# Kernel optimization log

Hardware: AMD Instinct MI355X
Metric: run time of the kernel (lower is better)

The kernel has to match this reference:

```python
import jax, jax.numpy as jnp
import numpy as np

EPS = 1e-6
H = 16  # num_heads


def _layernorm(x):
    m = jnp.mean(x, axis=-1, keepdims=True)
    v = jnp.mean((x - m) ** 2, axis=-1, keepdims=True)
    return (x - m) * jax.lax.rsqrt(v + EPS)


def _rmsnorm(x, scale):
    return x * jax.lax.rsqrt(jnp.mean(x * x, axis=-1, keepdims=True) + EPS) * scale


def _modulation(vec, w, b):
    # vec: [B, D] -> 6 tensors of [B, 1, D]
    out = jax.nn.silu(vec) @ w + b
    return jnp.split(out[:, None, :], 6, axis=-1)


def _qkv_heads(x, w):
    # x: [B, L, D] -> q,k,v each [B, H, L, Dh]  (rearrange 'B L (K H D) -> K B H L D')
    B, L, _ = x.shape
    qkv = (x @ w).reshape(B, L, 3, H, -1)
    qkv = jnp.transpose(qkv, (2, 0, 3, 1, 4))
    return qkv[0], qkv[1], qkv[2]


def _apply_rope(xq, xk, pe):
    # pe: [B, 1, L, Dh//2, 2, 2]
    shp = xq.shape
    xq_ = xq.reshape(*shp[:-1], -1, 1, 2)
    xk_ = xk.reshape(*shp[:-1], -1, 1, 2)
    xq_out = pe[..., 0] * xq_[..., 0] + pe[..., 1] * xq_[..., 1]
    xk_out = pe[..., 0] * xk_[..., 0] + pe[..., 1] * xk_[..., 1]
    return xq_out.reshape(shp), xk_out.reshape(shp)


def _attention(q, k, v, pe):
    q, k = _apply_rope(q, k, pe)
    scale = q.shape[-1] ** -0.5
    logits = jnp.einsum('bhqd,bhkd->bhqk', q, k) * scale
    probs = jax.nn.softmax(logits, axis=-1)
    x = jnp.einsum('bhqk,bhkd->bhqd', probs, v)
    B, h, L, Dh = x.shape
    return jnp.transpose(x, (0, 2, 1, 3)).reshape(B, L, h * Dh)


def reference(obs, cond, vec, pe,
              obs_mod_w, obs_mod_b, obs_qkv_w, obs_q_scale, obs_k_scale,
              obs_proj_w, obs_proj_b, obs_mlp_w1, obs_mlp_b1, obs_mlp_w2, obs_mlp_b2,
              cond_mod_w, cond_mod_b, cond_qkv_w, cond_q_scale, cond_k_scale,
              cond_proj_w, cond_proj_b, cond_mlp_w1, cond_mlp_b1, cond_mlp_w2, cond_mlp_b2):
    o_shift1, o_scale1, o_gate1, o_shift2, o_scale2, o_gate2 = _modulation(vec, obs_mod_w, obs_mod_b)
    c_shift1, c_scale1, c_gate1, c_shift2, c_scale2, c_gate2 = _modulation(vec, cond_mod_w, cond_mod_b)

    obs_m = (1 + o_scale1) * _layernorm(obs) + o_shift1
    oq, ok, ov = _qkv_heads(obs_m, obs_qkv_w)
    oq = _rmsnorm(oq, obs_q_scale)
    ok = _rmsnorm(ok, obs_k_scale)

    cond_m = (1 + c_scale1) * _layernorm(cond) + c_shift1
    cq, ck, cv = _qkv_heads(cond_m, cond_qkv_w)
    cq = _rmsnorm(cq, cond_q_scale)
    ck = _rmsnorm(ck, cond_k_scale)

    q = jnp.concatenate((cq, oq), axis=2)
    k = jnp.concatenate((ck, ok), axis=2)
    v = jnp.concatenate((cv, ov), axis=2)
    attn = _attention(q, k, v, pe)
    Lc = cond.shape[1]
    cond_attn, obs_attn = attn[:, :Lc], attn[:, Lc:]

    obs = obs + o_gate1 * (obs_attn @ obs_proj_w + obs_proj_b)
    h_obs = (1 + o_scale2) * _layernorm(obs) + o_shift2
    obs = obs + o_gate2 * (jax.nn.gelu(h_obs @ obs_mlp_w1 + obs_mlp_b1, approximate=True) @ obs_mlp_w2 + obs_mlp_b2)

    cond = cond + c_gate1 * (cond_attn @ cond_proj_w + cond_proj_b)
    h_cond = (1 + c_scale2) * _layernorm(cond) + c_shift2
    cond = cond + c_gate2 * (jax.nn.gelu(h_cond @ cond_mlp_w1 + cond_mlp_b1, approximate=True) @ cond_mlp_w2 + cond_mlp_b2)
    return obs, cond


def setup_inputs() -> dict:
    key = jax.random.key(0)
    ks = jax.random.split(key, 24)
    D, Dh, Mh = 1024, 64, 4096
    Lo, Lc = 3072, 1024
    B = 1
    s = 0.02
    inp = {
        'obs': jax.random.normal(ks[0], (B, Lo, D), jnp.float32),
        'cond': jax.random.normal(ks[1], (B, Lc, D), jnp.float32),
        'vec': jax.random.normal(ks[2], (B, D), jnp.float32),
        'pe': jax.random.normal(ks[3], (B, 1, Lo + Lc, Dh // 2, 2, 2), jnp.float32),
        'obs_mod_w': jax.random.normal(ks[4], (D, 6 * D), jnp.float32) * s,
        'obs_mod_b': jax.random.normal(ks[5], (6 * D,), jnp.float32) * s,
        'obs_qkv_w': jax.random.normal(ks[6], (D, 3 * D), jnp.float32) * s,
        'obs_q_scale': jnp.ones((Dh,), jnp.float32),
        'obs_k_scale': jnp.ones((Dh,), jnp.float32),
        'obs_proj_w': jax.random.normal(ks[7], (D, D), jnp.float32) * s,
        'obs_proj_b': jax.random.normal(ks[8], (D,), jnp.float32) * s,
        'obs_mlp_w1': jax.random.normal(ks[9], (D, Mh), jnp.float32) * s,
        'obs_mlp_b1': jax.random.normal(ks[10], (Mh,), jnp.float32) * s,
        'obs_mlp_w2': jax.random.normal(ks[11], (Mh, D), jnp.float32) * s,
        'obs_mlp_b2': jax.random.normal(ks[12], (D,), jnp.float32) * s,
        'cond_mod_w': jax.random.normal(ks[13], (D, 6 * D), jnp.float32) * s,
        'cond_mod_b': jax.random.normal(ks[14], (6 * D,), jnp.float32) * s,
        'cond_qkv_w': jax.random.normal(ks[15], (D, 3 * D), jnp.float32) * s,
        'cond_q_scale': jnp.ones((Dh,), jnp.float32),
        'cond_k_scale': jnp.ones((Dh,), jnp.float32),
        'cond_proj_w': jax.random.normal(ks[16], (D, D), jnp.float32) * s,
        'cond_proj_b': jax.random.normal(ks[17], (D,), jnp.float32) * s,
        'cond_mlp_w1': jax.random.normal(ks[18], (D, Mh), jnp.float32) * s,
        'cond_mlp_b1': jax.random.normal(ks[19], (Mh,), jnp.float32) * s,
        'cond_mlp_w2': jax.random.normal(ks[20], (Mh, D), jnp.float32) * s,
        'cond_mlp_b2': jax.random.normal(ks[21], (D,), jnp.float32) * s,
    }
    return inp
```

## Files before the change

### kernel.cpp

```cpp
#include <hip/hip_runtime.h>

typedef unsigned short u16;
typedef __bf16 bf16x8 __attribute__((ext_vector_type(8)));
typedef __bf16 bf16x4 __attribute__((ext_vector_type(4)));
typedef float f32x4 __attribute__((ext_vector_type(4)));

#define GLOAD_LDS16(g, l)                                                    \
  __builtin_amdgcn_global_load_lds(                                          \
      (const __attribute__((address_space(1))) void*)(g),                    \
      (__attribute__((address_space(3))) void*)(l), 16, 0, 0)

__device__ __forceinline__ u16 f2bf(float f) {
  unsigned int u = __float_as_uint(f);
  u += 0x7fffu + ((u >> 16) & 1u);
  return (u16)(u >> 16);
}
__device__ __forceinline__ float bf2f(u16 h) {
  return __uint_as_float(((unsigned int)h) << 16);
}
__device__ __forceinline__ unsigned int pack_bf2(float a, float b) {
  return (__float_as_uint(b) & 0xffff0000u) | (__float_as_uint(a) >> 16);
}
__device__ __forceinline__ float fexp2(float x) {
#if __has_builtin(__builtin_amdgcn_exp2f)
  return __builtin_amdgcn_exp2f(x);
#else
  return exp2f(x);
#endif
}
__device__ __forceinline__ float gelu_tanh(float x) {
  float u = 0.7978845608028654f * (x + 0.044715f * x * x * x);
  float e = fexp2(-2.8853900817779268f * fabsf(u));
  float t = (1.0f - e) / (1.0f + e);
  t = (u >= 0.0f) ? t : -t;
  return 0.5f * x * (1.0f + t);
}
__device__ __forceinline__ float silu_f(float v) {
  return v / (1.0f + fexp2(-1.4426950408889634f * v));
}
__device__ __forceinline__ f32x4 mfma16(bf16x8 a, bf16x8 b, f32x4 c) {
  return __builtin_amdgcn_mfma_f32_16x16x32_bf16(a, b, c, 0, 0, 0);
}
__device__ __forceinline__ bf16x8 ld8u(const u16* p) {
  bf16x4 a = *(const bf16x4*)p;
  bf16x4 b = *(const bf16x4*)(p + 4);
  return __builtin_shufflevector(a, b, 0, 1, 2, 3, 4, 5, 6, 7);
}

__global__ __launch_bounds__(256) void modulation_kernel(
    const float* __restrict__ vec,
    const float* __restrict__ w_o, const float* __restrict__ b_o,
    const float* __restrict__ w_c, const float* __restrict__ b_c,
    float* __restrict__ o_mod, float* __restrict__ c_mod) {
  __shared__ float sv[1024];
  __shared__ float red[256];
  const int tid = threadIdx.x;
  const bool isobs = blockIdx.x < 96;
  const float* w = isobs ? w_o : w_c;
  const float* b = isobs ? b_o : b_c;
  float* out = isobs ? o_mod : c_mod;
  const int jb = (isobs ? blockIdx.x : blockIdx.x - 96) * 64;
  const int col = tid & 63, sl = tid >> 6;
  for (int i = tid; i < 1024; i += 256) {
    sv[i] = silu_f(vec[i]);
  }
  __syncthreads();
  float acc = 0.0f;
  const int kb = sl * 256;
  for (int k = 0; k < 256; ++k)
    acc += sv[kb + k] * w[(size_t)(kb + k) * 6144 + jb + col];
  red[tid] = acc;
  __syncthreads();
  if (sl == 0)
    out[jb + col] = red[col] + red[col + 64] + red[col + 128] + red[col + 192] + b[jb + col];
}

__global__ __launch_bounds__(256) void ln_mod_kernel(
    const float* __restrict__ xc, const float* __restrict__ xo,
    const float* __restrict__ modc, const float* __restrict__ modo,
    int mod_off, u16* __restrict__ out) {
  const int row = blockIdx.x, tid = threadIdx.x;
  const bool is_c = row < 1024;
  const float* x = is_c ? (xc + (size_t)row * 1024) : (xo + (size_t)(row - 1024) * 1024);
  const float* mod = (is_c ? modc : modo) + mod_off;
  float4 v = *(const float4*)(x + tid * 4);
  float s1 = v.x + v.y + v.z + v.w;
  float s2 = v.x * v.x + v.y * v.y + v.z * v.z + v.w * v.w;
#pragma unroll
  for (int m = 1; m < 64; m <<= 1) {
    s1 += __shfl_xor(s1, m);
    s2 += __shfl_xor(s2, m);
  }
  __shared__ float red[8];
  const int w = tid >> 6;
  if ((tid & 63) == 0) { red[w] = s1; red[4 + w] = s2; }
  __syncthreads();
  s1 = red[0] + red[1] + red[2] + red[3];
  s2 = red[4] + red[5] + red[6] + red[7];
  const float mean = s1 * (1.0f / 1024.0f);
  const float var = s2 * (1.0f / 1024.0f) - mean * mean;
  const float rstd = rsqrtf(var + 1e-6f);
  const int d = tid * 4;
  float vv[4] = {v.x, v.y, v.z, v.w};
  ushort4 ov;
  u16* po = (u16*)&ov;
#pragma unroll
  for (int i = 0; i < 4; ++i) {
    float y = (vv[i] - mean) * rstd;
    po[i] = f2bf((1.0f + mod[1024 + d + i]) * y + mod[d + i]);
  }
  *(ushort4*)(out + (size_t)row * 1024 + d) = ov;
}

__global__ __launch_bounds__(256) void ln_mod_b_kernel(
    const u16* __restrict__ x,
    const float* __restrict__ modc, const float* __restrict__ modo,
    int mod_off, u16* __restrict__ out) {
  const int row = blockIdx.x, tid = threadIdx.x;
  const bool is_c = row < 1024;
  const float* mod = (is_c ? modc : modo) + mod_off;
  ushort4 rv = *(const ushort4*)(x + (size_t)row * 1024 + tid * 4);
  float vv[4] = {bf2f(rv.x), bf2f(rv.y), bf2f(rv.z), bf2f(rv.w)};
  float s1 = vv[0] + vv[1] + vv[2] + vv[3];
  float s2 = vv[0] * vv[0] + vv[1] * vv[1] + vv[2] * vv[2] + vv[3] * vv[3];
#pragma unroll
  for (int m = 1; m < 64; m <<= 1) {
    s1 += __shfl_xor(s1, m);
    s2 += __shfl_xor(s2, m);
  }
  __shared__ float red[8];
  const int w = tid >> 6;
  if ((tid & 63) == 0) { red[w] = s1; red[4 + w] = s2; }
  __syncthreads();
  s1 = red[0] + red[1] + red[2] + red[3];
  s2 = red[4] + red[5] + red[6] + red[7];
  const float mean = s1 * (1.0f / 1024.0f);
  const float var = s2 * (1.0f / 1024.0f) - mean * mean;
  const float rstd = rsqrtf(var + 1e-6f);
  const int d = tid * 4;
  ushort4 ov;
  u16* po = (u16*)&ov;
#pragma unroll
  for (int i = 0; i < 4; ++i) {
    float y = (vv[i] - mean) * rstd;
    po[i] = f2bf((1.0f + mod[1024 + d + i]) * y + mod[d + i]);
  }
  *(ushort4*)(out + (size_t)row * 1024 + d) = ov;
}

__global__ __launch_bounds__(256) void transcast_kernel(
    const float* __restrict__ src_c, const float* __restrict__ src_o,
    u16* __restrict__ dst_c, u16* __restrict__ dst_o, int K, int N) {
  const float* src = blockIdx.z ? src_o : src_c;
  u16* dst = blockIdx.z ? dst_o : dst_c;
  const int n0 = blockIdx.x * 64, k0 = blockIdx.y * 64;
  __shared__ float s[64][65];
  const int tid = threadIdx.x;
  const int r = tid >> 4, c4 = (tid & 15) << 2;
#pragma unroll
  for (int p = 0; p < 4; ++p) {
    int kk = r + p * 16;
    float4 v = *(const float4*)(src + (size_t)(k0 + kk) * N + n0 + c4);
    s[kk][c4] = v.x; s[kk][c4 + 1] = v.y; s[kk][c4 + 2] = v.z; s[kk][c4 + 3] = v.w;
  }
  __syncthreads();
#pragma unroll
  for (int p = 0; p < 4; ++p) {
    int nr = r + p * 16;
    ushort4 ov;
    ov.x = f2bf(s[c4 + 0][nr]); ov.y = f2bf(s[c4 + 1][nr]);
    ov.z = f2bf(s[c4 + 2][nr]); ov.w = f2bf(s[c4 + 3][nr]);
    *(ushort4*)(dst + (size_t)(n0 + nr) * K + k0 + c4) = ov;
  }
}

template <int BN>
__global__ __launch_bounds__(256) void gemm_bf16(
    const u16* __restrict__ A, const u16* __restrict__ BTc, const u16* __restrict__ BTo,
    int N, int K, int mode,
    const float* __restrict__ bias_c, const float* __restrict__ bias_o,
    const float* __restrict__ gate_c, const float* __restrict__ gate_o,
    const float* __restrict__ x0_c, const float* __restrict__ x0_o,
    const u16* __restrict__ x1, void* __restrict__ outp,
    u16* __restrict__ oq, u16* __restrict__ ok, u16* __restrict__ ov) {
  constexpr int MI = (BN == 128) ? 4 : 2;
  __shared__ u16 As[128 * 32];
  __shared__ u16 Bs[BN * 32];
  const int tid = threadIdx.x;
  const int m0 = blockIdx.y * 128, n0 = blockIdx.x * BN;
  const bool is_c = (m0 < 1024);
  const u16* __restrict__ BT = is_c ? BTc : BTo;
  const int w = tid >> 6, lane = tid & 63, quad = lane >> 4, ln = lane & 15;
  const int wm = (BN == 128) ? (w >> 1) * 64 : w * 32;
  const int wn = (BN == 128) ? (w & 1) * 64 : 0;
  f32x4 acc[MI][4] = {};
  const int nkt = K >> 5;
  for (int kt = 0; kt < nkt; ++kt) {
    __syncthreads();
    {
      int c = tid;
      GLOAD_LDS16(A + (size_t)(m0 + (c >> 2)) * K + kt * 32 + (c & 3) * 8, As + c * 8);
      c = tid + 256;
      GLOAD_LDS16(A + (size_t)(m0 + (c >> 2)) * K + kt * 32 + (c & 3) * 8, As + c * 8);
      c = tid;
      GLOAD_LDS16(BT + (size_t)(n0 + (c >> 2)) * K + kt * 32 + (c & 3) * 8, Bs + c * 8);
      if (BN == 128) {
        c = tid + 256;
        GLOAD_LDS16(BT + (size_t)(n0 + (c >> 2)) * K + kt * 32 + (c & 3) * 8, Bs + c * 8);
      }
    }
    __syncthreads();
    bf16x8 a[MI], b[4];
#pragma unroll
    for (int i = 0; i < MI; ++i)
      a[i] = *(const bf16x8*)(As + (wm + i * 16 + ln) * 32 + quad * 8);
#pragma unroll
    for (int j = 0; j < 4; ++j)
      b[j] = *(const bf16x8*)(Bs + (wn + j * 16 + ln) * 32 + quad * 8);
#pragma unroll
    for (int i = 0; i < MI; ++i)
#pragma unroll
      for (int j = 0; j < 4; ++j) acc[i][j] = mfma16(a[i], b[j], acc[i][j]);
  }
  const float* bias = is_c ? bias_c : bias_o;
  const float* gate = is_c ? gate_c : gate_o;
  const float* x0 = is_c ? x0_c : x0_o;
#pragma unroll
  for (int i = 0; i < MI; ++i) {
#pragma unroll
    for (int j = 0; j < 4; ++j) {
#pragma unroll
      for (int r = 0; r < 4; ++r) {
        const int row = m0 + wm + i * 16 + quad * 4 + r;
        const int col = n0 + wn + j * 16 + ln;
        const float v = acc[i][j][r];
        if (mode == 0) {
          const int which = col >> 10, hh = (col & 1023) >> 6, dd = col & 63;
          u16* dst = (which == 0) ? oq : (which == 1) ? ok : ov;
          dst[((size_t)hh * 4096 + row) * 64 + dd] = f2bf(v);
        } else if (mode == 1) {
          const float xv = is_c ? x0[(size_t)row * 1024 + col]
                                : x0[(size_t)(row - 1024) * 1024 + col];
          ((u16*)outp)[(size_t)row * 1024 + col] = f2bf(xv + gate[col] * (v + bias[col]));
        } else if (mode == 2) {
          ((u16*)outp)[(size_t)row * N + col] = f2bf(gelu_tanh(v + bias[col]));
        } else {
          const float res = bf2f(x1[(size_t)row * 1024 + col]);
          const float val = res + gate[col] * (v + bias[col]);
          const size_t oidx = (row < 1024)
              ? (size_t)3145728 + (size_t)row * 1024 + col
              : (size_t)(row - 1024) * 1024 + col;
          ((float*)outp)[oidx] = val;
        }
      }
    }
  }
}

__global__ __launch_bounds__(256) void qkprep_kernel(
    const float* __restrict__ pe,
    const float* __restrict__ qs_c, const float* __restrict__ ks_c,
    const float* __restrict__ qs_o, const float* __restrict__ ks_o,
    u16* __restrict__ qraw, u16* __restrict__ kraw) {
  const int l = blockIdx.x, tid = threadIdx.x;
  const bool is_c = l < 1024;
  const float* qs = is_c ? qs_c : qs_o;
  const float* ks = is_c ? ks_c : ks_o;
  const int head = tid >> 4, dd = (tid * 4) & 63;
  const size_t off = ((size_t)head * 4096 + l) * 64 + dd;
  const float* peb = pe + (size_t)l * 128 + (size_t)dd * 2;
  float4 pe0 = *(const float4*)(peb);
  float4 pe1 = *(const float4*)(peb + 4);
  {
    ushort4 raw = *(const ushort4*)(qraw + off);
    float x0 = bf2f(raw.x), x1v = bf2f(raw.y), x2 = bf2f(raw.z), x3 = bf2f(raw.w);
    float ssq = x0 * x0 + x1v * x1v + x2 * x2 + x3 * x3;
#pragma unroll
    for (int m = 1; m < 16; m <<= 1) ssq += __shfl_xor(ssq, m);
    float rms = rsqrtf(ssq * (1.0f / 64.0f) + 1e-6f) * 0.18033688011112042f;
    float n0 = x0 * rms * qs[dd + 0], n1 = x1v * rms * qs[dd + 1];
    float n2 = x2 * rms * qs[dd + 2], n3 = x3 * rms * qs[dd + 3];
    ushort4 o;
    o.x = f2bf(pe0.x * n0 + pe0.y * n1);
    o.y = f2bf(pe0.z * n0 + pe0.w * n1);
    o.z = f2bf(pe1.x * n2 + pe1.y * n3);
    o.w = f2bf(pe1.z * n2 + pe1.w * n3);
    *(ushort4*)(qraw + off) = o;
  }
  {
    ushort4 raw = *(const ushort4*)(kraw + off);
    float x0 = bf2f(raw.x), x1v = bf2f(raw.y), x2 = bf2f(raw.z), x3 = bf2f(raw.w);
    float ssq = x0 * x0 + x1v * x1v + x2 * x2 + x3 * x3;
#pragma unroll
    for (int m = 1; m < 16; m <<= 1) ssq += __shfl_xor(ssq, m);
    float rms = rsqrtf(ssq * (1.0f / 64.0f) + 1e-6f);
    float n0 = x0 * rms * ks[dd + 0], n1 = x1v * rms * ks[dd + 1];
    float n2 = x2 * rms * ks[dd + 2], n3 = x3 * rms * ks[dd + 3];
    ushort4 o;
    o.x = f2bf(pe0.x * n0 + pe0.y * n1);
    o.y = f2bf(pe0.z * n0 + pe0.w * n1);
    o.z = f2bf(pe1.x * n2 + pe1.y * n3);
    o.w = f2bf(pe1.z * n2 + pe1.w * n3);
    *(ushort4*)(kraw + off) = o;
  }
}

__global__ __launch_bounds__(256) void vtrans_kernel(
    const u16* __restrict__ vh, u16* __restrict__ vt) {
  const int h = blockIdx.y, k0 = blockIdx.x * 64;
  __shared__ u16 s[64 * 66];
  const int tid = threadIdx.x;
#pragma unroll
  for (int st = 0; st < 2; ++st) {
    int c = tid + st * 256;
    int row = c >> 3, off = (c & 7) << 3;
    ushort4 v0 = *(const ushort4*)(vh + ((size_t)h * 4096 + k0 + row) * 64 + off);
    ushort4 v1 = *(const ushort4*)(vh + ((size_t)h * 4096 + k0 + row) * 64 + off + 4);
    u16* p = s + row * 66 + off;
    p[0] = v0.x; p[1] = v0.y; p[2] = v0.z; p[3] = v0.w;
    p[4] = v1.x; p[5] = v1.y; p[6] = v1.z; p[7] = v1.w;
  }
  __syncthreads();
#pragma unroll
  for (int st = 0; st < 2; ++st) {
    int c = tid + st * 256;
    int dd = c >> 3, kk = (c & 7) << 3;
    ushort4 a, b;
    a.x = s[(kk + 0) * 66 + dd]; a.y = s[(kk + 1) * 66 + dd];
    a.z = s[(kk + 2) * 66 + dd]; a.w = s[(kk + 3) * 66 + dd];
    b.x = s[(kk + 4) * 66 + dd]; b.y = s[(kk + 5) * 66 + dd];
    b.z = s[(kk + 6) * 66 + dd]; b.w = s[(kk + 7) * 66 + dd];
    u16* o = vt + ((size_t)h * 64 + dd) * 4096 + k0 + kk;
    *(ushort4*)(o) = a;
    *(ushort4*)(o + 4) = b;
  }
}

__device__ __forceinline__ void attn_chunk(
    int cn, const u16* kbase, const u16* vbase, u16* Pw,
    int w, int ln, int quad,
    const bf16x8 (&bq)[4][2],
    bf16x8 (&akc)[2][2], bf16x8 (&bvc)[4],
    bf16x8 (&akn)[2][2], bf16x8 (&bvn)[4],
    f32x4 (&o)[4][4], float (&rs)[4]) {
  constexpr int L = 4096;
  if (cn < 32) {
    const int kbn = cn * 128 + w * 32;
#pragma unroll
    for (int kk = 0; kk < 2; ++kk)
#pragma unroll
      for (int hf = 0; hf < 2; ++hf)
        akn[kk][hf] = *(const bf16x8*)(kbase + (size_t)(kbn + kk * 16 + ln) * 64 + hf * 32 + quad * 8);
#pragma unroll
    for (int jd = 0; jd < 4; ++jd)
      bvn[jd] = *(const bf16x8*)(vbase + (size_t)(jd * 16 + ln) * L + kbn + quad * 8);
  }
  f32x4 sT[2][4] = {};
#pragma unroll
  for (int kk = 0; kk < 2; ++kk)
#pragma unroll
    for (int nq = 0; nq < 4; ++nq) {
      sT[kk][nq] = mfma16(akc[kk][0], bq[nq][0], sT[kk][nq]);
      sT[kk][nq] = mfma16(akc[kk][1], bq[nq][1], sT[kk][nq]);
    }
#pragma unroll
  for (int kk = 0; kk < 2; ++kk)
#pragma unroll
    for (int nq = 0; nq < 4; ++nq) {
      float p0 = fexp2(sT[kk][nq][0]);
      float p1 = fexp2(sT[kk][nq][1]);
      float p2 = fexp2(sT[kk][nq][2]);
      float p3 = fexp2(sT[kk][nq][3]);
      rs[nq] += (p0 + p1) + (p2 + p3);
      uint2 pk;
      pk.x = pack_bf2(p0, p1);
      pk.y = pack_bf2(p2, p3);
      *(uint2*)(Pw + (nq * 16 + ln) * 36 + kk * 16 + quad * 4) = pk;
    }
  bf16x8 ap[4];
#pragma unroll
  for (int nq = 0; nq < 4; ++nq)
    ap[nq] = ld8u(Pw + (nq * 16 + ln) * 36 + quad * 8);
#pragma unroll
  for (int jd = 0; jd < 4; ++jd)
#pragma unroll
    for (int nq = 0; nq < 4; ++nq)
      o[nq][jd] = mfma16(ap[nq], bvc[jd], o[nq][jd]);
}

__global__ __launch_bounds__(256) void attn_kernel(
    const u16* __restrict__ qh, const u16* __restrict__ kh,
    const u16* __restrict__ vt, u16* __restrict__ attn) {
  constexpr int L = 4096;
  const int h = blockIdx.y;
  const int q0 = blockIdx.x * 64;
  const int tid = threadIdx.x, w = tid >> 6, lane = tid & 63;
  const int quad = lane >> 4, ln = lane & 15;
  __shared__ __align__(16) char smem[35840];
  u16* Pw = (u16*)(smem) + (size_t)w * 2304;
  float* bufA = (float*)smem;
  float* bufB = bufA + 4352;
  float* rs4 = bufB + 4352;

  bf16x8 bq[4][2];
  const u16* qbase = qh + ((size_t)h * L + q0) * 64;
#pragma unroll
  for (int nq = 0; nq < 4; ++nq)
#pragma unroll
    for (int hf = 0; hf < 2; ++hf)
      bq[nq][hf] = *(const bf16x8*)(qbase + (nq * 16 + ln) * 64 + hf * 32 + quad * 8);

  f32x4 o[4][4] = {};
  float rs[4] = {0.f, 0.f, 0.f, 0.f};
  const u16* kbase = kh + (size_t)h * L * 64;
  const u16* vbase = vt + (size_t)h * 64 * L;

  bf16x8 akA[2][2], akB[2][2], bvA[4], bvB[4];
  {
    const int kb0 = w * 32;
#pragma unroll
    for (int kk = 0; kk < 2; ++kk)
#pragma unroll
      for (int hf = 0; hf < 2; ++hf)
        akA[kk][hf] = *(const bf16x8*)(kbase + (size_t)(kb0 + kk * 16 + ln) * 64 + hf * 32 + quad * 8);
#pragma unroll
    for (int jd = 0; jd < 4; ++jd)
      bvA[jd] = *(const bf16x8*)(vbase + (size_t)(jd * 16 + ln) * L + kb0 + quad * 8);
  }
  for (int c = 0; c < 32; c += 2) {
    attn_chunk(c + 1, kbase, vbase, Pw, w, ln, quad, bq, akA, bvA, akB, bvB, o, rs);
    attn_chunk(c + 2, kbase, vbase, Pw, w, ln, quad, bq, akB, bvB, akA, bvA, o, rs);
  }

  __syncthreads();
#pragma unroll
  for (int nq = 0; nq < 4; ++nq) {
    rs[nq] += __shfl_xor(rs[nq], 16);
    rs[nq] += __shfl_xor(rs[nq], 32);
  }
  if (quad == 0) {
#pragma unroll
    for (int nq = 0; nq < 4; ++nq) rs4[w * 64 + nq * 16 + ln] = rs[nq];
  }
  if (w == 1) {
#pragma unroll
    for (int nq = 0; nq < 4; ++nq)
#pragma unroll
      for (int jd = 0; jd < 4; ++jd)
        *(f32x4*)(bufA + (jd * 16 + ln) * 68 + nq * 16 + quad * 4) = o[nq][jd];
  }
  if (w == 3) {
#pragma unroll
    for (int nq = 0; nq < 4; ++nq)
#pragma unroll
      for (int jd = 0; jd < 4; ++jd)
        *(f32x4*)(bufB + (jd * 16 + ln) * 68 + nq * 16 + quad * 4) = o[nq][jd];
  }
  __syncthreads();
  if (w == 0) {
#pragma unroll
    for (int nq = 0; nq < 4; ++nq)
#pragma unroll
      for (int jd = 0; jd < 4; ++jd)
        o[nq][jd] += *(const f32x4*)(bufA + (jd * 16 + ln) * 68 + nq * 16 + quad * 4);
  }
  if (w == 2) {
#pragma unroll
    for (int nq = 0; nq < 4; ++nq)
#pragma unroll
      for (int jd = 0; jd < 4; ++jd)
        o[nq][jd] += *(const f32x4*)(bufB + (jd * 16 + ln) * 68 + nq * 16 + quad * 4);
  }
  __syncthreads();
  if (w == 2) {
#pragma unroll
    for (int nq = 0; nq < 4; ++nq)
#pragma unroll
      for (int jd = 0; jd < 4; ++jd)
        *(f32x4*)(bufA + (jd * 16 + ln) * 68 + nq * 16 + quad * 4) = o[nq][jd];
  }
  __syncthreads();
  if (w == 0) {
    float linv[4][4];
#pragma unroll
    for (int nq = 0; nq < 4; ++nq)
#pragma unroll
      for (int r = 0; r < 4; ++r) {
        const int qr = nq * 16 + quad * 4 + r;
        linv[nq][r] = 1.0f / (rs4[qr] + rs4[64 + qr] + rs4[128 + qr] + rs4[192 + qr]);
      }
#pragma unroll
    for (int nq = 0; nq < 4; ++nq)
#pragma unroll
      for (int jd = 0; jd < 4; ++jd) {
        f32x4 of = o[nq][jd];
        of += *(const f32x4*)(bufA + (jd * 16 + ln) * 68 + nq * 16 + quad * 4);
#pragma unroll
        for (int r = 0; r < 4; ++r) {
          const int row = q0 + nq * 16 + quad * 4 + r;
          attn[(size_t)row * 1024 + h * 64 + jd * 16 + ln] = f2bf(of[r] * linv[nq][r]);
        }
      }
  }
}

extern "C" void kernel_launch(void* const* d_in, const int* in_sizes, int n_in,
                              void* d_out, int out_size, void* d_ws, size_t ws_size,
                              hipStream_t stream) {
  (void)in_sizes; (void)n_in; (void)out_size; (void)ws_size;
  const float* obs         = (const float*)d_in[0];
  const float* cond        = (const float*)d_in[1];
  const float* vec         = (const float*)d_in[2];
  const float* pe          = (const float*)d_in[3];
  const float* obs_mod_w   = (const float*)d_in[4];
  const float* obs_mod_b   = (const float*)d_in[5];
  const float* obs_qkv_w   = (const float*)d_in[6];
  const float* obs_q_scale = (const float*)d_in[7];
  const float* obs_k_scale = (const float*)d_in[8];
  const float* obs_proj_w  = (const float*)d_in[9];
  const float* obs_proj_b  = (const float*)d_in[10];
  const float* obs_mlp_w1  = (const float*)d_in[11];
  const float* obs_mlp_b1  = (const float*)d_in[12];
  const float* obs_mlp_w2  = (const float*)d_in[13];
  const float* obs_mlp_b2  = (const float*)d_in[14];
  const float* cond_mod_w  = (const float*)d_in[15];
  const float* cond_mod_b  = (const float*)d_in[16];
  const float* cond_qkv_w  = (const float*)d_in[17];
  const float* cond_q_scale= (const float*)d_in[18];
  const float* cond_k_scale= (const float*)d_in[19];
  const float* cond_proj_w = (const float*)d_in[20];
  const float* cond_proj_b = (const float*)d_in[21];
  const float* cond_mlp_w1 = (const float*)d_in[22];
  const float* cond_mlp_b1 = (const float*)d_in[23];
  const float* cond_mlp_w2 = (const float*)d_in[24];
  const float* cond_mlp_b2 = (const float*)d_in[25];

  char* ws = (char*)d_ws;
  float* o_mod = (float*)ws;
  float* c_mod = o_mod + 6144;
  char* base = ws + 65536;
  u16* qkvT_c  = (u16*)base;
  u16* qkvT_o  = (u16*)(base + 6291456);
  u16* projT_c = (u16*)base;
  u16* projT_o = (u16*)(base + 2097152);
  u16* mlp1T_c = (u16*)base;
  u16* mlp1T_o = (u16*)(base + 8388608);
  u16* mlp2T_c = (u16*)base;
  u16* mlp2T_o = (u16*)(base + 8388608);
  u16* xm   = (u16*)(base + 16777216);
  u16* x1   = (u16*)(base + 16777216);
  u16* qraw = (u16*)(base + 25165824);
  u16* hm   = (u16*)(base + 25165824);
  u16* kraw = (u16*)(base + 33554432);
  u16* vraw = (u16*)(base + 41943040);
  u16* vt   = (u16*)(base + 50331648);
  u16* attn = (u16*)(base + 58720256);
  u16* g    = (u16*)(base + 33554432);

  modulation_kernel<<<192, 256, 0, stream>>>(vec, obs_mod_w, obs_mod_b,
                                             cond_mod_w, cond_mod_b, o_mod, c_mod);
  ln_mod_kernel<<<4096, 256, 0, stream>>>(cond, obs, c_mod, o_mod, 0, xm);
  transcast_kernel<<<dim3(48, 16, 2), 256, 0, stream>>>(cond_qkv_w, obs_qkv_w,
                                                        qkvT_c, qkvT_o, 1024, 3072);
  gemm_bf16<128><<<dim3(24, 32), 256, 0, stream>>>(xm, qkvT_c, qkvT_o, 3072, 1024, 0,
      nullptr, nullptr, nullptr, nullptr, nullptr, nullptr, nullptr, nullptr,
      qraw, kraw, vraw);
  qkprep_kernel<<<4096, 256, 0, stream>>>(pe, cond_q_scale, cond_k_scale,
                                          obs_q_scale, obs_k_scale, qraw, kraw);
  vtrans_kernel<<<dim3(64, 16), 256, 0, stream>>>(vraw, vt);
  attn_kernel<<<dim3(64, 16), 256, 0, stream>>>(qraw, kraw, vt, attn);
  transcast_kernel<<<dim3(16, 16, 2), 256, 0, stream>>>(cond_proj_w, obs_proj_w,
                                                        projT_c, projT_o, 1024, 1024);
  gemm_bf16<64><<<dim3(16, 32), 256, 0, stream>>>(attn, projT_c, projT_o, 1024, 1024, 1,
      cond_proj_b, obs_proj_b, c_mod + 2048, o_mod + 2048, cond, obs,
      nullptr, (void*)x1, nullptr, nullptr, nullptr);
  ln_mod_b_kernel<<<4096, 256, 0, stream>>>(x1, c_mod, o_mod, 3072, hm);
  transcast_kernel<<<dim3(64, 16, 2), 256, 0, stream>>>(cond_mlp_w1, obs_mlp_w1,
                                                        mlp1T_c, mlp1T_o, 1024, 4096);
  gemm_bf16<128><<<dim3(32, 32), 256, 0, stream>>>(hm, mlp1T_c, mlp1T_o, 4096, 1024, 2,
      cond_mlp_b1, obs_mlp_b1, nullptr, nullptr, nullptr, nullptr,
      nullptr, (void*)g, nullptr, nullptr, nullptr);
  transcast_kernel<<<dim3(16, 64, 2), 256, 0, stream>>>(cond_mlp_w2, obs_mlp_w2,
                                                        mlp2T_c, mlp2T_o, 4096, 1024);
  gemm_bf16<64><<<dim3(16, 32), 256, 0, stream>>>(g, mlp2T_c, mlp2T_o, 1024, 4096, 3,
      cond_mlp_b2, obs_mlp_b2, c_mod + 5120, o_mod + 5120, nullptr, nullptr,
      x1, d_out, nullptr, nullptr, nullptr);
}
```

Measured before the change: 649.9 us.

## Software-pipeline attention so QK^T of a chunk overlaps PV of the previous

Restructures the attention inner loop into a skewed pipeline: each step computes scores and exp for chunk c while the P·V MFMAs consume the probabilities and V fragments from chunk c-1, which were loaded from LDS at the end of the previous step. K and V prefetches are split and placed around the compute phases, and MFMA blocks are wrapped in s_setprio to favour matrix issue. Launch bounds now request 3 blocks per CU, which constrains register allocation. The extra live ap/bv registers and the tighter occupancy target risk register spills.

```diff
diff --git a/kernel.cpp b/kernel.cpp
--- a/kernel.cpp
+++ b/kernel.cpp
@@ -336,59 +336,71 @@
   }
 }
 
-__device__ __forceinline__ void attn_chunk(
+__device__ __forceinline__ void attn_step(
     int cn, const u16* kbase, const u16* vbase, u16* Pw,
     int w, int ln, int quad,
     const bf16x8 (&bq)[4][2],
-    bf16x8 (&akc)[2][2], bf16x8 (&bvc)[4],
-    bf16x8 (&akn)[2][2], bf16x8 (&bvn)[4],
+    bf16x8 (&akc)[2][2], bf16x8 (&akn)[2][2],
+    bf16x8 (&bvv)[4], bf16x8 (&ap)[4],
     f32x4 (&o)[4][4], float (&rs)[4]) {
   constexpr int L = 4096;
+  f32x4 sT[2][4] = {};
   if (cn < 32) {
-    const int kbn = cn * 128 + w * 32;
+    if (cn + 1 < 32) {
+      const int kbn = (cn + 1) * 128 + w * 32;
+#pragma unroll
+      for (int kk = 0; kk < 2; ++kk)
+#pragma unroll
+        for (int hf = 0; hf < 2; ++hf)
+          akn[kk][hf] = *(const bf16x8*)(kbase + (size_t)(kbn + kk * 16 + ln) * 64 + hf * 32 + quad * 8);
+    }
+    __builtin_amdgcn_s_setprio(1);
 #pragma unroll
     for (int kk = 0; kk < 2; ++kk)
 #pragma unroll
-      for (int hf = 0; hf < 2; ++hf)
-        akn[kk][hf] = *(const bf16x8*)(kbase + (size_t)(kbn + kk * 16 + ln) * 64 + hf * 32 + quad * 8);
+      for (int nq = 0; nq < 4; ++nq) {
+        sT[kk][nq] = mfma16(akc[kk][0], bq[nq][0], sT[kk][nq]);
+        sT[kk][nq] = mfma16(akc[kk][1], bq[nq][1], sT[kk][nq]);
+      }
+    __builtin_amdgcn_s_setprio(0);
+#pragma unroll
+    for (int kk = 0; kk < 2; ++kk)
+#pragma unroll
+      for (int nq = 0; nq < 4; ++nq) {
+        float p0 = fexp2(sT[kk][nq][0]);
+        float p1 = fexp2(sT[kk][nq][1]);
+        float p2 = fexp2(sT[kk][nq][2]);
+        float p3 = fexp2(sT[kk][nq][3]);
+        rs[nq] += (p0 + p1) + (p2 + p3);
+        uint2 pk;
+        pk.x = pack_bf2(p0, p1);
+        pk.y = pack_bf2(p2, p3);
+        *(uint2*)(Pw + (nq * 16 + ln) * 36 + kk * 16 + quad * 4) = pk;
+      }
+  }
+  if (cn > 0) {
+    __builtin_amdgcn_s_setprio(1);
 #pragma unroll
     for (int jd = 0; jd < 4; ++jd)
-      bvn[jd] = *(const bf16x8*)(vbase + (size_t)(jd * 16 + ln) * L + kbn + quad * 8);
-  }
-  f32x4 sT[2][4] = {};
-#pragma unroll
-  for (int kk = 0; kk < 2; ++kk)
-#pragma unroll
-    for (int nq = 0; nq < 4; ++nq) {
-      sT[kk][nq] = mfma16(akc[kk][0], bq[nq][0], sT[kk][nq]);
-      sT[kk][nq] = mfma16(akc[kk][1], bq[nq][1], sT[kk][nq]);
+#pragma unroll
+      for (int nq = 0; nq < 4; ++nq)
+        o[nq][jd] = mfma16(ap[nq], bvv[jd], o[nq][jd]);
+    __builtin_amdgcn_s_setprio(0);
+  }
+  if (cn < 32) {
+    if (cn + 1 < 32) {
+      const int kbn = (cn + 1) * 128 + w * 32;
+#pragma unroll
+      for (int jd = 0; jd < 4; ++jd)
+        bvv[jd] = *(const bf16x8*)(vbase + (size_t)(jd * 16 + ln) * L + kbn + quad * 8);
     }
 #pragma unroll
-  for (int kk = 0; kk < 2; ++kk)
-#pragma unroll
-    for (int nq = 0; nq < 4; ++nq) {
-      float p0 = fexp2(sT[kk][nq][0]);
-      float p1 = fexp2(sT[kk][nq][1]);
-      float p2 = fexp2(sT[kk][nq][2]);
-      float p3 = fexp2(sT[kk][nq][3]);
-      rs[nq] += (p0 + p1) + (p2 + p3);
-      uint2 pk;
-      pk.x = pack_bf2(p0, p1);
-      pk.y = pack_bf2(p2, p3);
-      *(uint2*)(Pw + (nq * 16 + ln) * 36 + kk * 16 + quad * 4) = pk;
-    }
-  bf16x8 ap[4];
-#pragma unroll
-  for (int nq = 0; nq < 4; ++nq)
-    ap[nq] = ld8u(Pw + (nq * 16 + ln) * 36 + quad * 8);
-#pragma unroll
-  for (int jd = 0; jd < 4; ++jd)
-#pragma unroll
-    for (int nq = 0; nq < 4; ++nq)
-      o[nq][jd] = mfma16(ap[nq], bvc[jd], o[nq][jd]);
-}
-
-__global__ __launch_bounds__(256) void attn_kernel(
+    for (int nq = 0; nq < 4; ++nq)
+      ap[nq] = ld8u(Pw + (nq * 16 + ln) * 36 + quad * 8);
+  }
+}
+
+__global__ __launch_bounds__(256, 3) void attn_kernel(
     const u16* __restrict__ qh, const u16* __restrict__ kh,
     const u16* __restrict__ vt, u16* __restrict__ attn) {
   constexpr int L = 4096;
@@ -415,7 +427,7 @@
   const u16* kbase = kh + (size_t)h * L * 64;
   const u16* vbase = vt + (size_t)h * 64 * L;
 
-  bf16x8 akA[2][2], akB[2][2], bvA[4], bvB[4];
+  bf16x8 akA[2][2], akB[2][2], bvA[4], bvB[4], ap[4];
   {
     const int kb0 = w * 32;
 #pragma unroll
@@ -427,9 +439,10 @@
     for (int jd = 0; jd < 4; ++jd)
       bvA[jd] = *(const bf16x8*)(vbase + (size_t)(jd * 16 + ln) * L + kb0 + quad * 8);
   }
-  for (int c = 0; c < 32; c += 2) {
-    attn_chunk(c + 1, kbase, vbase, Pw, w, ln, quad, bq, akA, bvA, akB, bvB, o, rs);
-    attn_chunk(c + 2, kbase, vbase, Pw, w, ln, quad, bq, akB, bvB, akA, bvA, o, rs);
+  attn_step(0, kbase, vbase, Pw, w, ln, quad, bq, akA, akB, bvB, ap, o, rs);
+  for (int c = 1; c < 32; c += 2) {
+    attn_step(c,     kbase, vbase, Pw, w, ln, quad, bq, akB, akA, bvA, ap, o, rs);
+    attn_step(c + 1, kbase, vbase, Pw, w, ln, quad, bq, akA, akB, bvB, ap, o, rs);
   }
 
   __syncthreads();
```

Result: slower. 988.9 us (+52.2%).

## Permute K row order so softmax probabilities feed PV MFMA directly from registers

Applied to the files above, without the earlier changes.

Each lane now loads K rows in a permuted order, so the S^T MFMA output layout lines up with the A-operand layout needed by the P·V MFMA. The probabilities are packed into registers and bit-cast straight into the MFMA operand, which removes the per-warp LDS write/read round trip for P. The cost is a less regular global access pattern for K and a tight dependence on the MFMA register-layout mapping being correct.

```diff
diff --git a/kernel.cpp b/kernel.cpp
--- a/kernel.cpp
+++ b/kernel.cpp
@@ -4,6 +4,7 @@
 typedef __bf16 bf16x8 __attribute__((ext_vector_type(8)));
 typedef __bf16 bf16x4 __attribute__((ext_vector_type(4)));
 typedef float f32x4 __attribute__((ext_vector_type(4)));
+typedef unsigned int u32x4 __attribute__((ext_vector_type(4)));
 
 #define GLOAD_LDS16(g, l)                                                    \
   __builtin_amdgcn_global_load_lds(                                          \
@@ -40,11 +41,6 @@
 }
 __device__ __forceinline__ f32x4 mfma16(bf16x8 a, bf16x8 b, f32x4 c) {
   return __builtin_amdgcn_mfma_f32_16x16x32_bf16(a, b, c, 0, 0, 0);
-}
-__device__ __forceinline__ bf16x8 ld8u(const u16* p) {
-  bf16x4 a = *(const bf16x4*)p;
-  bf16x4 b = *(const bf16x4*)(p + 4);
-  return __builtin_shufflevector(a, b, 0, 1, 2, 3, 4, 5, 6, 7);
 }
 
 __global__ __launch_bounds__(256) void modulation_kernel(
@@ -337,8 +333,8 @@
 }
 
 __device__ __forceinline__ void attn_chunk(
-    int cn, const u16* kbase, const u16* vbase, u16* Pw,
-    int w, int ln, int quad,
+    int cn, const u16* kbase, const u16* vbase,
+    int w, int ln, int quad, int kperm,
     const bf16x8 (&bq)[4][2],
     bf16x8 (&akc)[2][2], bf16x8 (&bvc)[4],
     bf16x8 (&akn)[2][2], bf16x8 (&bvn)[4],
@@ -350,7 +346,7 @@
     for (int kk = 0; kk < 2; ++kk)
 #pragma unroll
       for (int hf = 0; hf < 2; ++hf)
-        akn[kk][hf] = *(const bf16x8*)(kbase + (size_t)(kbn + kk * 16 + ln) * 64 + hf * 32 + quad * 8);
+        akn[kk][hf] = *(const bf16x8*)(kbase + (size_t)(kbn + kperm + kk * 4) * 64 + hf * 32 + quad * 8);
 #pragma unroll
     for (int jd = 0; jd < 4; ++jd)
       bvn[jd] = *(const bf16x8*)(vbase + (size_t)(jd * 16 + ln) * L + kbn + quad * 8);
@@ -364,28 +360,23 @@
       sT[kk][nq] = mfma16(akc[kk][1], bq[nq][1], sT[kk][nq]);
     }
 #pragma unroll
-  for (int kk = 0; kk < 2; ++kk)
-#pragma unroll
-    for (int nq = 0; nq < 4; ++nq) {
+  for (int nq = 0; nq < 4; ++nq) {
+    u32x4 pw;
+#pragma unroll
+    for (int kk = 0; kk < 2; ++kk) {
       float p0 = fexp2(sT[kk][nq][0]);
       float p1 = fexp2(sT[kk][nq][1]);
       float p2 = fexp2(sT[kk][nq][2]);
       float p3 = fexp2(sT[kk][nq][3]);
       rs[nq] += (p0 + p1) + (p2 + p3);
-      uint2 pk;
-      pk.x = pack_bf2(p0, p1);
-      pk.y = pack_bf2(p2, p3);
-      *(uint2*)(Pw + (nq * 16 + ln) * 36 + kk * 16 + quad * 4) = pk;
+      pw[kk * 2 + 0] = pack_bf2(p0, p1);
+      pw[kk * 2 + 1] = pack_bf2(p2, p3);
     }
-  bf16x8 ap[4];
-#pragma unroll
-  for (int nq = 0; nq < 4; ++nq)
-    ap[nq] = ld8u(Pw + (nq * 16 + ln) * 36 + quad * 8);
-#pragma unroll
-  for (int jd = 0; jd < 4; ++jd)
-#pragma unroll
-    for (int nq = 0; nq < 4; ++nq)
-      o[nq][jd] = mfma16(ap[nq], bvc[jd], o[nq][jd]);
+    const bf16x8 ap = __builtin_bit_cast(bf16x8, pw);
+#pragma unroll
+    for (int jd = 0; jd < 4; ++jd)
+      o[nq][jd] = mfma16(ap, bvc[jd], o[nq][jd]);
+  }
 }
 
 __global__ __launch_bounds__(256) void attn_kernel(
@@ -397,7 +388,6 @@
   const int tid = threadIdx.x, w = tid >> 6, lane = tid & 63;
   const int quad = lane >> 4, ln = lane & 15;
   __shared__ __align__(16) char smem[35840];
-  u16* Pw = (u16*)(smem) + (size_t)w * 2304;
   float* bufA = (float*)smem;
   float* bufB = bufA + 4352;
   float* rs4 = bufB + 4352;
@@ -414,6 +404,7 @@
   float rs[4] = {0.f, 0.f, 0.f, 0.f};
   const u16* kbase = kh + (size_t)h * L * 64;
   const u16* vbase = vt + (size_t)h * 64 * L;
+  const int kperm = ((ln >> 2) << 3) + (ln & 3);
 
   bf16x8 akA[2][2], akB[2][2], bvA[4], bvB[4];
   {
@@ -422,14 +413,14 @@
     for (int kk = 0; kk < 2; ++kk)
 #pragma unroll
       for (int hf = 0; hf < 2; ++hf)
-        akA[kk][hf] = *(const bf16x8*)(kbase + (size_t)(kb0 + kk * 16 + ln) * 64 + hf * 32 + quad * 8);
+        akA[kk][hf] = *(const bf16x8*)(kbase + (size_t)(kb0 + kperm + kk * 4) * 64 + hf * 32 + quad * 8);
 #pragma unroll
     for (int jd = 0; jd < 4; ++jd)
       bvA[jd] = *(const bf16x8*)(vbase + (size_t)(jd * 16 + ln) * L + kb0 + quad * 8);
   }
   for (int c = 0; c < 32; c += 2) {
-    attn_chunk(c + 1, kbase, vbase, Pw, w, ln, quad, bq, akA, bvA, akB, bvB, o, rs);
-    attn_chunk(c + 2, kbase, vbase, Pw, w, ln, quad, bq, akB, bvB, akA, bvA, o, rs);
+    attn_chunk(c + 1, kbase, vbase, w, ln, quad, kperm, bq, akA, bvA, akB, bvB, o, rs);
+    attn_chunk(c + 2, kbase, vbase, w, ln, quad, kperm, bq, akB, bvB, akA, bvA, o, rs);
   }
 
   __syncthreads();
```

New measurement: 648.4 us. Within noise of the previous version (-0.2%).
